# Kernel tuning notes

Measured on AMD Instinct MI355X. Metric: run time of the kernel, lower is better.

The kernel has to match this reference:

```python
import jax, jax.numpy as jnp
import numpy as np

T, B, H, NH = 1024, 4, 1024, 16
D = H // NH


def setup_inputs() -> dict:
    key = jax.random.key(0)
    ks = jax.random.split(key, 8)
    s = 0.02
    return {
        "x": jax.random.normal(ks[0], (T, B, H), jnp.float32),
        "pos": jax.random.normal(ks[1], (2 * T - 1, 1, H), jnp.float32),
        "attn_mask": jnp.zeros((T, T), jnp.bool_),
        "ln_w": jnp.ones((H,), jnp.float32),
        "ln_b": jnp.zeros((H,), jnp.float32),
        "in_proj_w": jax.random.normal(ks[2], (3 * H, H), jnp.float32) * s,
        "in_proj_b": jnp.zeros((3 * H,), jnp.float32),
        "pos_proj_w": jax.random.normal(ks[3], (H, H), jnp.float32) * s,
        "r_w_bias": jax.random.normal(ks[4], (NH, D), jnp.float32) * s,
        "r_r_bias": jax.random.normal(ks[5], (NH, D), jnp.float32) * s,
        "out_proj_w": jax.random.normal(ks[6], (H, H), jnp.float32) * s,
        "out_proj_b": jnp.zeros((H,), jnp.float32),
    }


def _layer_norm(x, w, b, eps=1e-5):
    m = jnp.mean(x, axis=-1, keepdims=True)
    v = jnp.var(x, axis=-1, keepdims=True)
    return (x - m) * jax.lax.rsqrt(v + eps) * w + b


def _rel_shift(x):
    # x: [qlen, 2*qlen-1, B, NH] -> Transformer-XL relative shift
    q = x.shape[0]
    zero_pad = jnp.zeros((q, 1) + x.shape[2:], x.dtype)
    xp = jnp.concatenate([zero_pad, x], axis=1)            # [q, 2q, B, NH]
    xp = xp.reshape((x.shape[1] + 1, q) + x.shape[2:])     # [2q, q, B, NH]
    return xp[1:].reshape(x.shape)                         # [q, 2q-1, B, NH]


def reference(x, pos, attn_mask, ln_w, ln_b, in_proj_w, in_proj_b,
              pos_proj_w, r_w_bias, r_r_bias, out_proj_w, out_proj_b):
    # pre-norm
    qn = _layer_norm(x, ln_w, ln_b)                        # [T,B,H]
    # fused qkv projection
    qkv = qn @ in_proj_w.T + in_proj_b                     # [T,B,3H]
    q, k, v = jnp.split(qkv, 3, axis=-1)
    q = q.reshape(T, B, NH, D)
    k = k.reshape(T, B, NH, D)
    v = v.reshape(T, B, NH, D)
    # relative position keys (bias-free projection)
    r = (pos[:, 0] @ pos_proj_w.T).reshape(2 * T - 1, NH, D)
    # content term (AC) and position term (BD), Transformer-XL style
    AC = jnp.einsum('ibnd,jbnd->ijbn', q + r_w_bias, k)    # [T,T,B,NH]
    BD = jnp.einsum('ibnd,jnd->ijbn', q + r_r_bias, r)     # [T,2T-1,B,NH]
    BD = _rel_shift(BD)[:, :T]                             # [T,T,B,NH]
    scale = 1.0 / np.sqrt(D).astype(np.float32)
    score = (AC + BD) * scale
    score = jnp.where(attn_mask[:, :, None, None], -jnp.inf, score)
    p = jax.nn.softmax(score, axis=1)                      # coverage
    out = jnp.einsum('ijbn,jbnd->ibnd', p, v).reshape(T, B, H)
    o = out @ out_proj_w.T + out_proj_b                    # residual dropout = identity (eval)
    return o
```

## Files before the change

### kernel.cpp

```cpp
#include <hip/hip_runtime.h>
#include <hip/hip_bf16.h>
#include <math.h>

#define T_DIM 1024
#define B_DIM 4
#define H_DIM 1024
#define NHEAD 16
#define DHEAD 64
#define NROWS (T_DIM * B_DIM)
#define LPOS  (2 * T_DIM - 1)
#define QS    (3 * H_DIM)

typedef __attribute__((ext_vector_type(8))) short bfrag;
typedef __attribute__((ext_vector_type(4))) short sh4;
typedef __attribute__((ext_vector_type(4))) float facc;

static __device__ __forceinline__ short f2bf(float f) {
    return __builtin_bit_cast(short, __float2bfloat16(f));
}
static __device__ __forceinline__ float bf2f(short s) {
    unsigned u = ((unsigned)(unsigned short)s) << 16;
    return __builtin_bit_cast(float, u);
}

#define GLD16(g, l) __builtin_amdgcn_global_load_lds( \
    (const __attribute__((address_space(1))) void*)(g), \
    (__attribute__((address_space(3))) void*)(l), 16, 0, 0)

__global__ __launch_bounds__(256) void prep_kernel(
    const float* __restrict__ x, const float* __restrict__ lnw,
    const float* __restrict__ lnb, short* __restrict__ qn,
    const float* __restrict__ s0, short* __restrict__ d0, int c0,
    const float* __restrict__ s1, short* __restrict__ d1, int c1,
    const float* __restrict__ s2, short* __restrict__ d2, int c2,
    const float* __restrict__ s3, short* __restrict__ d3, int c3) {
    __shared__ float red0[4], red1[4];
    const int bid = blockIdx.x;
    const int tid = threadIdx.x;
    if (bid < NROWS) {
        const float* xr = x + (size_t)bid * H_DIM;
        short* yr = qn + (size_t)bid * H_DIM;
        float4 v = reinterpret_cast<const float4*>(xr)[tid];
        float s  = v.x + v.y + v.z + v.w;
        float sq = v.x * v.x + v.y * v.y + v.z * v.z + v.w * v.w;
        #pragma unroll
        for (int m = 32; m; m >>= 1) {
            s  += __shfl_xor(s, m);
            sq += __shfl_xor(sq, m);
        }
        int wave = tid >> 6, lane = tid & 63;
        if (lane == 0) { red0[wave] = s; red1[wave] = sq; }
        __syncthreads();
        float tot   = red0[0] + red0[1] + red0[2] + red0[3];
        float totsq = red1[0] + red1[1] + red1[2] + red1[3];
        float mean = tot * (1.0f / H_DIM);
        float var  = totsq * (1.0f / H_DIM) - mean * mean;
        float rstd = rsqrtf(var + 1e-5f);
        float4 wv = reinterpret_cast<const float4*>(lnw)[tid];
        float4 bv = reinterpret_cast<const float4*>(lnb)[tid];
        sh4 o;
        o[0] = f2bf((v.x - mean) * rstd * wv.x + bv.x);
        o[1] = f2bf((v.y - mean) * rstd * wv.y + bv.y);
        o[2] = f2bf((v.z - mean) * rstd * wv.z + bv.z);
        o[3] = f2bf((v.w - mean) * rstd * wv.w + bv.w);
        reinterpret_cast<sh4*>(yr)[tid] = o;
    } else {
        int i = (bid - NROWS) * 256 + tid;
        const float* s; short* d; int off;
        if      (i < c0)                { s = s0; d = d0; off = i; }
        else if (i < c0 + c1)           { s = s1; d = d1; off = i - c0; }
        else if (i < c0 + c1 + c2)      { s = s2; d = d2; off = i - c0 - c1; }
        else if (i < c0 + c1 + c2 + c3) { s = s3; d = d3; off = i - c0 - c1 - c2; }
        else return;
        const float* sp = s + (size_t)off * 8;
        float4 a = *(const float4*)(sp);
        float4 b = *(const float4*)(sp + 4);
        bfrag f;
        f[0] = f2bf(a.x); f[1] = f2bf(a.y); f[2] = f2bf(a.z); f[3] = f2bf(a.w);
        f[4] = f2bf(b.x); f[5] = f2bf(b.y); f[6] = f2bf(b.z); f[7] = f2bf(b.w);
        *(bfrag*)(d + (size_t)off * 8) = f;
    }
}

template<int MODE>
static __device__ __forceinline__ void gemm_body(
    const short* __restrict__ A, const short* __restrict__ B,
    const float* __restrict__ bias, void* __restrict__ Cv,
    int M, int N, int K, int gx, int nblk, int bid,
    short (*As)[64], short (*Bs)[64]) {
    const int tid = threadIdx.x;
    const int w4 = tid >> 6, l = tid & 63;
    const int lc = l & 15, lg = l >> 4;
    const int wr = w4 >> 1, wc = w4 & 1;

    const int cpx = nblk >> 3;
    const int nl = (bid & 7) * cpx + (bid >> 3);
    const int row0 = (nl / gx) * 128, col0 = (nl % gx) * 128;

    const int srow = l >> 3;
    const int schunk = ((l & 7) ^ srow) * 8;
    const int Mm1 = M - 1;

    facc acc[4][4];
    #pragma unroll
    for (int i = 0; i < 4; ++i)
        #pragma unroll
        for (int j = 0; j < 4; ++j) acc[i][j] = (facc){0.f, 0.f, 0.f, 0.f};

    for (int k0 = 0; k0 < K; k0 += 64) {
        #pragma unroll
        for (int p = 0; p < 4; ++p) {
            int rA = p * 32 + w4 * 8 + srow;
            int ga = row0 + rA; if (ga > Mm1) ga = Mm1;
            GLD16(A + (size_t)ga * K + k0 + schunk,
                  (char*)As + p * 4096 + w4 * 1024);
            GLD16(B + (size_t)(col0 + rA) * K + k0 + schunk,
                  (char*)Bs + p * 4096 + w4 * 1024);
        }
        __syncthreads();

        bfrag af[4][2], bfr[4][2];
        #pragma unroll
        for (int fr = 0; fr < 4; ++fr) {
            const int ra = wr * 64 + fr * 16 + lc;
            #pragma unroll
            for (int ks = 0; ks < 2; ++ks)
                af[fr][ks] = *(const bfrag*)&As[ra][(((ks * 4 + lg) ^ (ra & 7)) << 3)];
        }
        #pragma unroll
        for (int fc = 0; fc < 4; ++fc) {
            const int rb = wc * 64 + fc * 16 + lc;
            #pragma unroll
            for (int ks = 0; ks < 2; ++ks)
                bfr[fc][ks] = *(const bfrag*)&Bs[rb][(((ks * 4 + lg) ^ (rb & 7)) << 3)];
        }
        #pragma unroll
        for (int fr = 0; fr < 4; ++fr)
            #pragma unroll
            for (int fc = 0; fc < 4; ++fc)
                #pragma unroll
                for (int ks = 0; ks < 2; ++ks)
                    acc[fr][fc] = __builtin_amdgcn_mfma_f32_16x16x32_bf16(
                        af[fr][ks], bfr[fc][ks], acc[fr][fc], 0, 0, 0);
        __syncthreads();
    }

    #pragma unroll
    for (int fc = 0; fc < 4; ++fc) {
        const int gc = col0 + wc * 64 + fc * 16 + lc;
        const float bv = bias ? bias[gc] : 0.f;
        #pragma unroll
        for (int fr = 0; fr < 4; ++fr) {
            #pragma unroll
            for (int rg = 0; rg < 4; ++rg) {
                const int gr = row0 + wr * 64 + fr * 16 + lg * 4 + rg;
                if (gr < M) {
                    float o = acc[fr][fc][rg] + bv;
                    if constexpr (MODE == 0) ((float*)Cv)[(size_t)gr * N + gc] = o;
                    else                     ((short*)Cv)[(size_t)gr * N + gc] = f2bf(o);
                }
            }
        }
    }
}

__global__ __launch_bounds__(256) void gemm_dual(
    const short* __restrict__ A0, const short* __restrict__ B0,
    const float* __restrict__ bias0, short* __restrict__ C0,
    const short* __restrict__ A1, const short* __restrict__ B1,
    short* __restrict__ C1) {
    __shared__ short As[128][64];
    __shared__ short Bs[128][64];
    const int bid = blockIdx.x;
    if (bid < 768)
        gemm_body<1>(A0, B0, bias0, C0, NROWS, QS, H_DIM, QS / 128, 768, bid, As, Bs);
    else
        gemm_body<1>(A1, B1, nullptr, C1, LPOS, H_DIM, H_DIM, H_DIM / 128, 128, bid - 768, As, Bs);
}

__global__ __launch_bounds__(256) void gemm_f32out(
    const short* __restrict__ A, const short* __restrict__ B,
    const float* __restrict__ bias, float* __restrict__ C) {
    __shared__ short As[128][64];
    __shared__ short Bs[128][64];
    gemm_body<0>(A, B, bias, C, NROWS, H_DIM, H_DIM, H_DIM / 128, 256, blockIdx.x, As, Bs);
}

__global__ __launch_bounds__(256) void vtrans_kernel(const short* __restrict__ qkv,
                                                     short* __restrict__ vT) {
    __shared__ short T[64][72];
    const int tt = blockIdx.x, hh = blockIdx.y, b = blockIdx.z;
    const int tid = threadIdx.x;
    const int w = tid >> 6, lane = tid & 63;

    const int tg = tt * 64 + lane;
    const short* src = qkv + (size_t)(tg * B_DIM + b) * QS + 2 * H_DIM + hh * 64 + w * 16;
    bfrag v0 = *(const bfrag*)(src);
    bfrag v1 = *(const bfrag*)(src + 8);
    #pragma unroll
    for (int e = 0; e < 8; ++e) T[w * 16 + e][lane] = v0[e];
    #pragma unroll
    for (int e = 0; e < 8; ++e) T[w * 16 + 8 + e][lane] = v1[e];
    __syncthreads();

    const int hd = tid >> 2, tc = tid & 3;
    bfrag o0 = *(const bfrag*)&T[hd][tc * 16];
    bfrag o1 = *(const bfrag*)&T[hd][tc * 16 + 8];
    short* dst = vT + (((size_t)(b * H_DIM + hh * 64 + hd)) << 10) + tt * 64 + tc * 16;
    *(bfrag*)(dst) = o0;
    *(bfrag*)(dst + 8) = o1;
}

__global__ __launch_bounds__(512, 4) void attn_mfma(const short* __restrict__ qkv,
                                                    const short* __restrict__ r,
                                                    const short* __restrict__ vt,
                                                    const float* __restrict__ rwb,
                                                    const float* __restrict__ rrb,
                                                    short* __restrict__ out) {
    __shared__ short Ks[64][64];
    __shared__ short Vt[64][64];
    __shared__ short Rs[192][64];
    __shared__ short BDPs[8][16][84];

    const int d_   = blockIdx.x;
    const int slot = d_ >> 3, xcd = d_ & 7;
    const int bn   = xcd + 8 * (slot >> 3);
    const int i0   = (slot & 7) * 128;
    const int b    = bn >> 4;
    const int n    = bn & 15;

    const int tid = threadIdx.x;
    const int w   = tid >> 6;
    const int l   = tid & 63;
    const int lg  = l >> 4;
    const int lc  = l & 15;
    const int hoff = n * DHEAD;

    const int srow8 = l >> 3;
    const int sc8   = ((l & 7) ^ srow8) * 8;

    bfrag qw[2], qr[2];
    {
        const int row = i0 + 16 * w + lc;
        const short* qrow = qkv + (size_t)(row * B_DIM + b) * QS + hoff;
        #pragma unroll
        for (int ks = 0; ks < 2; ++ks) {
            const int d0 = ks * 32 + lg * 8;
            bfrag qv = *(const bfrag*)(qrow + d0);
            float4 wa = *(const float4*)(rwb + hoff + d0);
            float4 wb = *(const float4*)(rwb + hoff + d0 + 4);
            float4 ra = *(const float4*)(rrb + hoff + d0);
            float4 rb = *(const float4*)(rrb + hoff + d0 + 4);
            const float sc = 0.125f * 1.44269504f;
            float wf[8] = {wa.x, wa.y, wa.z, wa.w, wb.x, wb.y, wb.z, wb.w};
            float rf[8] = {ra.x, ra.y, ra.z, ra.w, rb.x, rb.y, rb.z, rb.w};
            bfrag fw, fr;
            #pragma unroll
            for (int e = 0; e < 8; ++e) {
                float qf = bf2f(qv[e]);
                fw[e] = f2bf((qf + wf[e]) * sc);
                fr[e] = f2bf((qf + rf[e]) * sc);
            }
            qw[ks] = fw; qr[ks] = fr;
        }
    }

    facc ofr[4];
    #pragma unroll
    for (int d = 0; d < 4; ++d) ofr[d] = (facc){0.f, 0.f, 0.f, 0.f};
    float lrow[4] = {0.f, 0.f, 0.f, 0.f};
    const int wbase = 16 * (7 - w);
    const int base0 = 896 - i0;

    const short* kp = qkv + ((size_t)(w * 8 + srow8) * B_DIM + b) * QS + H_DIM + hoff + sc8;
    const short* vp = vt + (((size_t)(b * H_DIM + hoff + w * 8 + srow8)) << 10) + sc8;
    const size_t kstep = (size_t)64 * B_DIM * QS;
    bfrag* const ksd = (bfrag*)((char*)Ks + w * 1024 + l * 16);
    bfrag* const vtd = (bfrag*)((char*)Vt + w * 1024 + l * 16);

    bfrag stK, stV, stR;

    {
        stK = *(const bfrag*)(kp);
        stV = *(const bfrag*)(vp);
        bfrag r3[3];
        #pragma unroll
        for (int p = 0; p < 3; ++p) {
            int lrw = base0 + (w * 3 + p) * 8 + srow8;
            if (lrw > 2046) lrw = 2046;
            r3[p] = *(const bfrag*)(r + (size_t)lrw * H_DIM + hoff + sc8);
        }
        *ksd = stK;
        *vtd = stV;
        #pragma unroll
        for (int p = 0; p < 3; ++p)
            *(bfrag*)((char*)Rs + (w * 3 + p) * 1024 + l * 16) = r3[p];
    }
    __syncthreads();

    int off = 0;

    for (int jt = 0; jt < 16; ++jt) {
        if (jt < 15) {
            stK = *(const bfrag*)(kp + (size_t)(jt + 1) * kstep);
            stV = *(const bfrag*)(vp + (jt + 1) * 64);
            int lrw = base0 + jt * 64 + 192 + w * 8 + srow8;
            if (lrw > 2046) lrw = 2046;
            stR = *(const bfrag*)(r + (size_t)lrw * H_DIM + hoff + sc8);
        }

        __builtin_amdgcn_s_setprio(1);
        facc sfr[4];
        #pragma unroll
        for (int js = 0; js < 4; ++js) {
            sfr[js] = (facc){-4.f, -4.f, -4.f, -4.f};
            const int jrow = js * 16 + lc;
            #pragma unroll
            for (int ks = 0; ks < 2; ++ks) {
                const int ch = (ks * 4 + lg) ^ (jrow & 7);
                bfrag bf = *(const bfrag*)&Ks[jrow][ch << 3];
                sfr[js] = __builtin_amdgcn_mfma_f32_16x16x32_bf16(qw[ks], bf, sfr[js], 0, 0, 0);
            }
        }
        #pragma unroll
        for (int ls = 0; ls < 5; ++ls) {
            facc bd = (facc){-4.f, -4.f, -4.f, -4.f};
            const int rrow = wbase + ls * 16 + lc;
            int pr = rrow + off; if (pr >= 192) pr -= 192;
            #pragma unroll
            for (int ks = 0; ks < 2; ++ks) {
                const int ch = (ks * 4 + lg) ^ (rrow & 7);
                bfrag bf = *(const bfrag*)&Rs[pr][ch << 3];
                bd = __builtin_amdgcn_mfma_f32_16x16x32_bf16(qr[ks], bf, bd, 0, 0, 0);
            }
            #pragma unroll
            for (int rg = 0; rg < 4; ++rg)
                BDPs[w][lg * 4 + rg][ls * 16 + lc] = f2bf(bd[rg]);
        }
        __builtin_amdgcn_s_setprio(0);

        #pragma unroll
        for (int js = 0; js < 4; ++js)
            #pragma unroll
            for (int rg = 0; rg < 4; ++rg) {
                const int irow = lg * 4 + rg;
                float v = sfr[js][rg] + bf2f(BDPs[w][irow][js * 16 + lc - irow + 15]);
                float p = exp2f(v);
                lrow[rg] += p;
                BDPs[w][irow][js * 16 + lc] = f2bf(p);
            }

        bfrag pf[2];
        #pragma unroll
        for (int ks = 0; ks < 2; ++ks)
            pf[ks] = *(const bfrag*)&BDPs[w][lc][ks * 32 + lg * 8];
        __builtin_amdgcn_s_setprio(1);
        #pragma unroll
        for (int d = 0; d < 4; ++d) {
            #pragma unroll
            for (int ks = 0; ks < 2; ++ks) {
                const int vr = d * 16 + lc;
                const int ch = (ks * 4 + lg) ^ (vr & 7);
                bfrag vf = *(const bfrag*)&Vt[vr][ch << 3];
                ofr[d] = __builtin_amdgcn_mfma_f32_16x16x32_bf16(pf[ks], vf, ofr[d], 0, 0, 0);
            }
        }
        __builtin_amdgcn_s_setprio(0);

        __syncthreads();
        if (jt < 15) {
            *ksd = stK;
            *vtd = stV;
            *(bfrag*)((char*)Rs + ((off >> 3) + w) * 1024 + l * 16) = stR;
            __syncthreads();
            off += 64; if (off == 192) off = 0;
        }
    }

    #pragma unroll
    for (int m = 1; m < 16; m <<= 1)
        #pragma unroll
        for (int rg = 0; rg < 4; ++rg)
            lrow[rg] += __shfl_xor(lrow[rg], m);

    #pragma unroll
    for (int rg = 0; rg < 4; ++rg) {
        const float inv = 1.0f / lrow[rg];
        const int row = i0 + 16 * w + lg * 4 + rg;
        short* orow = out + (size_t)(row * B_DIM + b) * H_DIM + hoff;
        #pragma unroll
        for (int d = 0; d < 4; ++d)
            orow[d * 16 + lc] = f2bf(ofr[d][rg] * inv);
    }
}

extern "C" void kernel_launch(void* const* d_in, const int* in_sizes, int n_in,
                              void* d_out, int out_size, void* d_ws, size_t ws_size,
                              hipStream_t stream) {
    const float* x          = (const float*)d_in[0];
    const float* pos        = (const float*)d_in[1];
    const float* ln_w       = (const float*)d_in[3];
    const float* ln_b       = (const float*)d_in[4];
    const float* in_proj_w  = (const float*)d_in[5];
    const float* in_proj_b  = (const float*)d_in[6];
    const float* pos_proj_w = (const float*)d_in[7];
    const float* r_w_bias   = (const float*)d_in[8];
    const float* r_r_bias   = (const float*)d_in[9];
    const float* out_proj_w = (const float*)d_in[10];
    const float* out_proj_b = (const float*)d_in[11];
    float* out = (float*)d_out;

    short* qn   = (short*)d_ws;
    short* qkv  = qn + (size_t)NROWS * H_DIM;
    short* rbuf = qkv + (size_t)NROWS * QS;
    short* wi   = rbuf + (size_t)2048 * H_DIM;
    short* wp   = wi + (size_t)QS * H_DIM;
    short* wo   = wp + (size_t)H_DIM * H_DIM;
    short* posb = wo + (size_t)H_DIM * H_DIM;
    short* vT   = posb + (size_t)2048 * H_DIM;

    const int c0 = (LPOS * H_DIM) / 8;
    const int c1 = (QS * H_DIM) / 8;
    const int c2 = (H_DIM * H_DIM) / 8;
    const int c3 = c2;
    const int nchunk = c0 + c1 + c2 + c3;
    const int cvtblk = (nchunk + 255) / 256;
    prep_kernel<<<NROWS + cvtblk, 256, 0, stream>>>(
        x, ln_w, ln_b, qn,
        pos, posb, c0, in_proj_w, wi, c1, pos_proj_w, wp, c2, out_proj_w, wo, c3);

    gemm_dual<<<768 + 128, 256, 0, stream>>>(qn, wi, in_proj_b, qkv, posb, wp, rbuf);

    vtrans_kernel<<<dim3(16, 16, 4), 256, 0, stream>>>(qkv, vT);

    attn_mfma<<<512, 512, 0, stream>>>(
        qkv, rbuf, vT, r_w_bias, r_r_bias, qn);

    gemm_f32out<<<256, 256, 0, stream>>>(qn, wo, out_proj_b, out);
}
```

Before: 161.0 us.

## Use dedicated 256x256 double-buffered GEMM kernel for QKV projection

Replaces the QKV portion of the combined dual GEMM with a new 256x256-tile kernel using 512 threads, double-buffered LDS staging via async global loads, MFMA issue interleaved with loads, and s_setprio scheduling hints. The position projection moves to its own 128-tile launch. The larger tiles raise arithmetic intensity and reduce global traffic per FLOP. In exchange, only 192 blocks fill the GPU, the kernel uses heavy LDS (128KB), and there is an extra kernel launch with serialized pos GEMM.

```diff
diff --git a/kernel.cpp b/kernel.cpp
--- a/kernel.cpp
+++ b/kernel.cpp
@@ -82,6 +82,152 @@
     }
 }
 
+__global__ __launch_bounds__(512, 2) void gemm256(const short* __restrict__ A,
+                                                  const short* __restrict__ B,
+                                                  const float* __restrict__ bias,
+                                                  short* __restrict__ C) {
+    __shared__ short As[2][256][64];
+    __shared__ short Bs[2][256][64];
+    const int tid = threadIdx.x;
+    const int w = tid >> 6, l = tid & 63;
+    const int lc = l & 15, lg = l >> 4;
+    const int wm = w >> 2, wn = w & 3;
+
+    const int bid = blockIdx.x;
+    const int nl = (bid & 7) * 24 + (bid >> 3);
+    const int row0 = (nl / 12) * 256, col0 = (nl % 12) * 256;
+
+    auto stage_half = [&](int kt, int bufi, int hf) {
+        const short* Base = (hf & 2) ? B : A;
+        const int r0 = (hf & 2) ? col0 : row0;
+        char* dst = (hf & 2) ? (char*)Bs[bufi] : (char*)As[bufi];
+        const int h = hf & 1;
+        #pragma unroll
+        for (int q = 0; q < 2; ++q) {
+            const int slot = q * 512 + tid;
+            const int row = slot >> 3;
+            const int ch = (slot & 7) ^ (row & 7);
+            GLD16(Base + (size_t)(r0 + h * 128 + row) * 1024 + kt * 64 + ch * 8,
+                  dst + h * 16384 + slot * 16);
+        }
+    };
+
+    facc acc[8][4];
+    #pragma unroll
+    for (int m = 0; m < 8; ++m)
+        #pragma unroll
+        for (int n = 0; n < 4; ++n) acc[m][n] = (facc){0.f, 0.f, 0.f, 0.f};
+
+    #pragma unroll
+    for (int hf = 0; hf < 4; ++hf) stage_half(0, 0, hf);
+    #pragma unroll
+    for (int hf = 0; hf < 4; ++hf) stage_half(1, 1, hf);
+    asm volatile("s_waitcnt vmcnt(8)" ::: "memory");
+    __builtin_amdgcn_s_barrier();
+    __builtin_amdgcn_sched_barrier(0);
+
+    for (int t = 0; t < 16; ++t) {
+        const int cur = t & 1;
+        bfrag af[8][2], bf[4][2];
+
+        #pragma unroll
+        for (int m = 0; m < 4; ++m) {
+            const int ra = wm * 128 + m * 16 + lc;
+            #pragma unroll
+            for (int ks = 0; ks < 2; ++ks)
+                af[m][ks] = *(const bfrag*)&As[cur][ra][(((ks * 4 + lg) ^ (ra & 7)) << 3)];
+        }
+        #pragma unroll
+        for (int n = 0; n < 2; ++n) {
+            const int rb = wn * 64 + n * 16 + lc;
+            #pragma unroll
+            for (int ks = 0; ks < 2; ++ks)
+                bf[n][ks] = *(const bfrag*)&Bs[cur][rb][(((ks * 4 + lg) ^ (rb & 7)) << 3)];
+        }
+        __builtin_amdgcn_s_setprio(1);
+        #pragma unroll
+        for (int m = 0; m < 4; ++m)
+            #pragma unroll
+            for (int n = 0; n < 2; ++n)
+                #pragma unroll
+                for (int ks = 0; ks < 2; ++ks)
+                    acc[m][n] = __builtin_amdgcn_mfma_f32_16x16x32_bf16(
+                        af[m][ks], bf[n][ks], acc[m][n], 0, 0, 0);
+        __builtin_amdgcn_s_setprio(0);
+
+        #pragma unroll
+        for (int m = 4; m < 8; ++m) {
+            const int ra = wm * 128 + m * 16 + lc;
+            #pragma unroll
+            for (int ks = 0; ks < 2; ++ks)
+                af[m][ks] = *(const bfrag*)&As[cur][ra][(((ks * 4 + lg) ^ (ra & 7)) << 3)];
+        }
+        #pragma unroll
+        for (int n = 2; n < 4; ++n) {
+            const int rb = wn * 64 + n * 16 + lc;
+            #pragma unroll
+            for (int ks = 0; ks < 2; ++ks)
+                bf[n][ks] = *(const bfrag*)&Bs[cur][rb][(((ks * 4 + lg) ^ (rb & 7)) << 3)];
+        }
+        __builtin_amdgcn_s_setprio(1);
+        #pragma unroll
+        for (int m = 4; m < 8; ++m)
+            #pragma unroll
+            for (int n = 0; n < 2; ++n)
+                #pragma unroll
+                for (int ks = 0; ks < 2; ++ks)
+                    acc[m][n] = __builtin_amdgcn_mfma_f32_16x16x32_bf16(
+                        af[m][ks], bf[n][ks], acc[m][n], 0, 0, 0);
+        __builtin_amdgcn_s_setprio(0);
+
+        __builtin_amdgcn_s_barrier();
+        __builtin_amdgcn_sched_barrier(0);
+
+        if (t + 2 < 16) { stage_half(t + 2, cur, 0); stage_half(t + 2, cur, 1); }
+        __builtin_amdgcn_s_setprio(1);
+        #pragma unroll
+        for (int m = 0; m < 4; ++m)
+            #pragma unroll
+            for (int n = 2; n < 4; ++n)
+                #pragma unroll
+                for (int ks = 0; ks < 2; ++ks)
+                    acc[m][n] = __builtin_amdgcn_mfma_f32_16x16x32_bf16(
+                        af[m][ks], bf[n][ks], acc[m][n], 0, 0, 0);
+        __builtin_amdgcn_s_setprio(0);
+
+        if (t + 2 < 16) { stage_half(t + 2, cur, 2); stage_half(t + 2, cur, 3); }
+        __builtin_amdgcn_s_setprio(1);
+        #pragma unroll
+        for (int m = 4; m < 8; ++m)
+            #pragma unroll
+            for (int n = 2; n < 4; ++n)
+                #pragma unroll
+                for (int ks = 0; ks < 2; ++ks)
+                    acc[m][n] = __builtin_amdgcn_mfma_f32_16x16x32_bf16(
+                        af[m][ks], bf[n][ks], acc[m][n], 0, 0, 0);
+        __builtin_amdgcn_s_setprio(0);
+
+        if (t + 2 < 16) asm volatile("s_waitcnt vmcnt(8)" ::: "memory");
+        else            asm volatile("s_waitcnt vmcnt(0)" ::: "memory");
+        __builtin_amdgcn_s_barrier();
+        __builtin_amdgcn_sched_barrier(0);
+    }
+
+    #pragma unroll
+    for (int n = 0; n < 4; ++n) {
+        const int gc = col0 + wn * 64 + n * 16 + lc;
+        const float bv = bias[gc];
+        #pragma unroll
+        for (int m = 0; m < 8; ++m) {
+            #pragma unroll
+            for (int rg = 0; rg < 4; ++rg) {
+                const int gr = row0 + wm * 128 + m * 16 + lg * 4 + rg;
+                C[(size_t)gr * 3072 + gc] = f2bf(acc[m][n][rg] + bv);
+            }
+        }
+    }
+}
+
 template<int MODE>
 static __device__ __forceinline__ void gemm_body(
     const short* __restrict__ A, const short* __restrict__ B,
@@ -164,18 +310,12 @@
     }
 }
 
-__global__ __launch_bounds__(256) void gemm_dual(
-    const short* __restrict__ A0, const short* __restrict__ B0,
-    const float* __restrict__ bias0, short* __restrict__ C0,
-    const short* __restrict__ A1, const short* __restrict__ B1,
-    short* __restrict__ C1) {
+__global__ __launch_bounds__(256) void gemm_pos(
+    const short* __restrict__ A, const short* __restrict__ B,
+    short* __restrict__ C) {
     __shared__ short As[128][64];
     __shared__ short Bs[128][64];
-    const int bid = blockIdx.x;
-    if (bid < 768)
-        gemm_body<1>(A0, B0, bias0, C0, NROWS, QS, H_DIM, QS / 128, 768, bid, As, Bs);
-    else
-        gemm_body<1>(A1, B1, nullptr, C1, LPOS, H_DIM, H_DIM, H_DIM / 128, 128, bid - 768, As, Bs);
+    gemm_body<1>(A, B, nullptr, C, LPOS, H_DIM, H_DIM, H_DIM / 128, 128, blockIdx.x, As, Bs);
 }
 
 __global__ __launch_bounds__(256) void gemm_f32out(
@@ -429,7 +569,9 @@
         x, ln_w, ln_b, qn,
         pos, posb, c0, in_proj_w, wi, c1, pos_proj_w, wp, c2, out_proj_w, wo, c3);
 
-    gemm_dual<<<768 + 128, 256, 0, stream>>>(qn, wi, in_proj_b, qkv, posb, wp, rbuf);
+    gemm256<<<192, 512, 0, stream>>>(qn, wi, in_proj_b, qkv);
+
+    gemm_pos<<<128, 256, 0, stream>>>(posb, wp, rbuf);
 
     vtrans_kernel<<<dim3(16, 16, 4), 256, 0, stream>>>(qkv, vT);
 
```

After: 156.5 us. -2.8%, faster.
